# Kernel optimization log

Measured on AMD Instinct MI355X. Metric: run time of the kernel, lower is better.

## Reference

```python
import jax, jax.numpy as jnp
import numpy as np

NUM_PARAMS = 1024
BATCH = 65536


def build_lifted_core(rotation_params, diagonal_scaling_params, n):
    """Faithful translation of the torch forward's lifted-core construction."""
    h = n // 2
    dt = rotation_params.dtype
    # skew-symmetric matrix S[i,j] = r[i] - r[j]
    S = rotation_params[:, None] - rotation_params[None, :]
    I = jnp.eye(h, dtype=dt)
    # Cayley transform: (I - S)^{-1} (I + S)
    rotation = jnp.linalg.solve(I - S, I + S)
    # core = diag(d) @ rotation  (row scaling)
    core = diagonal_scaling_params[:, None] * rotation  # [h, h]
    # rot90 has period 4 in k -> precompute the 4 distinct rotated cores
    rots = jnp.stack([jnp.rot90(core, k=k) for k in range(4)])  # [4, h, h]

    def body(o, L):
        blk = jax.lax.dynamic_slice(L, (o, o), (h, h)) + rots[o % 4]
        return jax.lax.dynamic_update_slice(L, blk, (o, o))

    lifted = jax.lax.fori_loop(0, h + 1, body, jnp.zeros((n, n), dtype=dt))
    return lifted


def setup_inputs() -> dict:
    key = jax.random.key(0)
    k1, k2, k3 = jax.random.split(key, 3)
    x = jax.random.normal(k1, (BATCH, NUM_PARAMS), dtype=jnp.float32)
    rotation_params = jax.random.normal(k2, (NUM_PARAMS // 2,), dtype=jnp.float32)
    diagonal_scaling_params = jax.random.normal(k3, (NUM_PARAMS // 2,), dtype=jnp.float32)
    return {"x": x, "rotation_params": rotation_params,
            "diagonal_scaling_params": diagonal_scaling_params}


def reference(x, rotation_params, diagonal_scaling_params):
    n = x.shape[-1]
    lifted = build_lifted_core(rotation_params, diagonal_scaling_params, n)
    return x @ lifted.T
```

## Files before the change

kernel.cpp:

```cpp
#include <hip/hip_runtime.h>
#include <hip/hip_bf16.h>

typedef __attribute__((ext_vector_type(8))) short sh8;
typedef __attribute__((ext_vector_type(4))) float f32x4;
typedef unsigned short u16;
typedef unsigned int u32;

#define GLOAD16(g, l)                                                          \
  __builtin_amdgcn_global_load_lds((const __attribute__((address_space(1))) u32*)(g), \
                                   (__attribute__((address_space(3))) u32*)(l), 16, 0, 0)

__global__ __launch_bounds__(512) void prep_kernel(const float* __restrict__ r,
                                                   const float* __restrict__ d,
                                                   float* __restrict__ pq) {
  int t = threadIdx.x;
  float rv = r[t], dv = d[t];
  float s1 = rv, s2 = rv * rv;
#pragma unroll
  for (int off = 32; off; off >>= 1) {
    s1 += __shfl_down(s1, off);
    s2 += __shfl_down(s2, off);
  }
  __shared__ float a1[8], a2[8];
  if ((t & 63) == 0) { a1[t >> 6] = s1; a2[t >> 6] = s2; }
  __syncthreads();
  float S1 = 0.f, S2 = 0.f;
#pragma unroll
  for (int w = 0; w < 8; ++w) { S1 += a1[w]; S2 += a2[w]; }
  float delta = 1.f - S1 * S1 + 512.f * S2;
  float c = 2.f / delta;
  pq[t]       = c * dv * ((1.f + S1) * rv - S2);
  pq[512 + t] = -c * dv * (512.f * rv + 1.f - S1);
}

__global__ __launch_bounds__(256) void build_lifted(const float* __restrict__ rg,
                                                    const float* __restrict__ dg,
                                                    const float* __restrict__ pq,
                                                    u16* __restrict__ Lhi,
                                                    u16* __restrict__ Llo) {
  __shared__ float r[512], d[512], p[512], q[512];
  int t = threadIdx.x;
  for (int k = t; k < 512; k += 256) {
    r[k] = rg[k]; d[k] = dg[k]; p[k] = pq[k]; q[k] = pq[512 + k];
  }
  __syncthreads();
  const int i = blockIdx.x >> 2;
  const int j = ((blockIdx.x & 3) << 8) | t;
  const int olo = max(0, max(i, j) - 511);
  const int ohi = min(min(i, j), 512);
  float val = 0.f;
  for (int o = olo + ((0 - olo) & 3); o <= ohi; o += 4) {
    int a = i - o; val += p[a] + q[a] * r[j - o];
  }
  for (int o = olo + ((1 - olo) & 3); o <= ohi; o += 4) {
    int a = j - o; val += p[a] + q[a] * r[511 - i + o];
  }
  for (int o = olo + ((2 - olo) & 3); o <= ohi; o += 4) {
    int a = 511 - i + o; val += p[a] + q[a] * r[511 - j + o];
  }
  for (int o = olo + ((3 - olo) & 3); o <= ohi; o += 4) {
    int a = 511 - j + o; val += p[a] + q[a] * r[i - o];
  }
  if (i == j) {
    for (int o = olo + ((0 - olo) & 3); o <= ohi; o += 4) val += d[i - o];
    for (int o = olo + ((2 - olo) & 3); o <= ohi; o += 4) val += d[511 - i + o];
  } else if ((i + j) & 1) {
    int os = (i + j - 511) >> 1;
    if (os >= olo && os <= ohi && (os & 1)) {
      int idx = ((os & 3) == 1) ? ((511 + j - i) >> 1) : ((511 + i - j) >> 1);
      val += d[idx];
    }
  }
  __hip_bfloat16 h = __float2bfloat16(val);
  float hf = __bfloat162float(h);
  __hip_bfloat16 l = __float2bfloat16(val - hf);
  size_t idx = ((size_t)((i >> 7) * 16 + (j >> 6)) << 13) + (size_t)((i & 127) << 6) +
               (size_t)((j & 63) ^ ((i & 7) << 3));
  union { __hip_bfloat16 b; u16 u; } ch, cl;
  ch.b = h; cl.b = l;
  Lhi[idx] = ch.u; Llo[idx] = cl.u;
}

__global__ __launch_bounds__(256, 2) void gemm_kernel(const float* __restrict__ x,
                                                      const u16* __restrict__ Bhg,
                                                      const u16* __restrict__ Blg,
                                                      float* __restrict__ out) {
  __shared__ u16 Ah[8192], Al[8192], Bh[8192], Bl[8192];
  const int tid = threadIdx.x;
  const int nb = blockIdx.x & 7;
  const int mb = blockIdx.x >> 3;
  const int m0 = mb << 7;
  const int n0 = nb << 7;
  const int lane = tid & 63;
  const int wave = tid >> 6;
  const int wm = wave >> 1, wn = wave & 1;
  const int lr = lane & 15, lg = lane >> 4;
  const int sel = (lr & 7) << 3;

  const int srow = tid >> 4;
  const int scol = (tid & 15) << 2;
  const int sidx0 = (srow << 6) + (scol ^ ((srow & 7) << 3));
  const float* xbase = x + (size_t)(m0 + srow) * 1024 + scol;

  f32x4 acc[4][4] = {};
  int baseA[4], baseB[4];
#pragma unroll
  for (int f = 0; f < 4; ++f) {
    baseA[f] = ((wm << 6) + (f << 4) + lr) << 6;
    baseB[f] = ((wn << 6) + (f << 4) + lr) << 6;
  }
  const u16* tBh = Bhg + ((size_t)nb << 17);
  const u16* tBl = Blg + ((size_t)nb << 17);

  for (int kt = 0; kt < 16; ++kt) {
    __syncthreads();
    {
      const u16* gh = tBh + (kt << 13) + (tid << 3);
      const u16* gl = tBl + (kt << 13) + (tid << 3);
#pragma unroll
      for (int c = 0; c < 4; ++c) {
        GLOAD16(gh + (c << 11), &Bh[(tid << 3) + (c << 11)]);
        GLOAD16(gl + (c << 11), &Bl[(tid << 3) + (c << 11)]);
      }
    }
    float4 av[8];
    const float* xp = xbase + (kt << 6);
#pragma unroll
    for (int cc = 0; cc < 8; ++cc)
      av[cc] = *reinterpret_cast<const float4*>(xp + (size_t)cc * 16 * 1024);
#pragma unroll
    for (int cc = 0; cc < 8; ++cc) {
      float4 v = av[cc];
      __hip_bfloat162 h01 = __float22bfloat162_rn(make_float2(v.x, v.y));
      __hip_bfloat162 h23 = __float22bfloat162_rn(make_float2(v.z, v.w));
      float l0 = v.x - __bfloat162float(h01.x);
      float l1 = v.y - __bfloat162float(h01.y);
      float l2 = v.z - __bfloat162float(h23.x);
      float l3 = v.w - __bfloat162float(h23.y);
      __hip_bfloat162 m01 = __float22bfloat162_rn(make_float2(l0, l1));
      __hip_bfloat162 m23 = __float22bfloat162_rn(make_float2(l2, l3));
      union { __hip_bfloat162 h; u32 u; } uh0, uh1, ul0, ul1;
      uh0.h = h01; uh1.h = h23; ul0.h = m01; ul1.h = m23;
      int widx = sidx0 + (cc << 10);
      *reinterpret_cast<uint2*>(&Ah[widx]) = make_uint2(uh0.u, uh1.u);
      *reinterpret_cast<uint2*>(&Al[widx]) = make_uint2(ul0.u, ul1.u);
    }
    __syncthreads();
#pragma unroll
    for (int ks = 0; ks < 2; ++ks) {
      const int co = ((ks << 5) + (lg << 3)) ^ sel;
      sh8 ah[4], al[4], bh[4], bl[4];
#pragma unroll
      for (int f = 0; f < 4; ++f) {
        ah[f] = *reinterpret_cast<const sh8*>(&Ah[baseA[f] + co]);
        al[f] = *reinterpret_cast<const sh8*>(&Al[baseA[f] + co]);
        bh[f] = *reinterpret_cast<const sh8*>(&Bh[baseB[f] + co]);
        bl[f] = *reinterpret_cast<const sh8*>(&Bl[baseB[f] + co]);
      }
#pragma unroll
      for (int fm = 0; fm < 4; ++fm)
#pragma unroll
        for (int fn = 0; fn < 4; ++fn) {
          acc[fm][fn] = __builtin_amdgcn_mfma_f32_16x16x32_bf16(ah[fm], bh[fn], acc[fm][fn], 0, 0, 0);
          acc[fm][fn] = __builtin_amdgcn_mfma_f32_16x16x32_bf16(ah[fm], bl[fn], acc[fm][fn], 0, 0, 0);
          acc[fm][fn] = __builtin_amdgcn_mfma_f32_16x16x32_bf16(al[fm], bh[fn], acc[fm][fn], 0, 0, 0);
        }
    }
  }
#pragma unroll
  for (int fm = 0; fm < 4; ++fm) {
    int row = m0 + (wm << 6) + (fm << 4) + (lg << 2);
#pragma unroll
    for (int fn = 0; fn < 4; ++fn) {
      int col = n0 + (wn << 6) + (fn << 4) + lr;
      float* op = out + (size_t)row * 1024 + col;
#pragma unroll
      for (int rr = 0; rr < 4; ++rr) op[(size_t)rr * 1024] = acc[fm][fn][rr];
    }
  }
}

extern "C" void kernel_launch(void* const* d_in, const int* in_sizes, int n_in,
                              void* d_out, int out_size, void* d_ws, size_t ws_size,
                              hipStream_t stream) {
  (void)in_sizes; (void)n_in; (void)out_size; (void)ws_size;
  const float* x  = (const float*)d_in[0];
  const float* r  = (const float*)d_in[1];
  const float* dg = (const float*)d_in[2];
  float* out = (float*)d_out;
  float* pq = (float*)d_ws;
  u16* Lhi = (u16*)((char*)d_ws + 4096);
  u16* Llo = Lhi + 1024 * 1024;

  prep_kernel<<<1, 512, 0, stream>>>(r, dg, pq);
  build_lifted<<<4096, 256, 0, stream>>>(r, dg, pq, Lhi, Llo);
  gemm_kernel<<<4096, 256, 0, stream>>>(x, Lhi, Llo, out);
}
```

Baseline: 769.1 us.

## Switch GEMM to fp16 two-term split and build lifted matrix via diagonal prefix sums

The GEMM now converts x to a single fp16 value and keeps a hi/lo fp16 split only for the lifted matrix. That cuts MFMA work from three products to two per tile, drops the Al shared buffer, and raises the occupancy hint to 3 blocks. The lifted-matrix builder now runs one block per diagonal and uses shared-memory prefix sums, so each entry costs a few lookups instead of an O(n) loop. The risk is lower accuracy: x loses its low-order correction term and fp16 has a narrower range than bf16.

```diff
diff --git a/kernel.cpp b/kernel.cpp
--- a/kernel.cpp
+++ b/kernel.cpp
@@ -1,7 +1,8 @@
 #include <hip/hip_runtime.h>
 #include <hip/hip_bf16.h>
-
-typedef __attribute__((ext_vector_type(8))) short sh8;
+#include <hip/hip_fp16.h>
+
+typedef __attribute__((ext_vector_type(8))) _Float16 h8;
 typedef __attribute__((ext_vector_type(4))) float f32x4;
 typedef unsigned short u16;
 typedef unsigned int u32;
@@ -33,59 +34,119 @@
   pq[512 + t] = -c * dv * (512.f * rv + 1.f - S1);
 }
 
-__global__ __launch_bounds__(256) void build_lifted(const float* __restrict__ rg,
-                                                    const float* __restrict__ dg,
-                                                    const float* __restrict__ pq,
-                                                    u16* __restrict__ Lhi,
-                                                    u16* __restrict__ Llo) {
-  __shared__ float r[512], d[512], p[512], q[512];
-  int t = threadIdx.x;
-  for (int k = t; k < 512; k += 256) {
-    r[k] = rg[k]; d[k] = dg[k]; p[k] = pq[k]; q[k] = pq[512 + k];
+__global__ __launch_bounds__(256) void build_lifted_diag(const float* __restrict__ rg,
+                                                         const float* __restrict__ dg,
+                                                         const float* __restrict__ pq,
+                                                         u16* __restrict__ Lhi,
+                                                         u16* __restrict__ Llo) {
+  __shared__ float r_s[512], d_s[512];
+  __shared__ float W[6][512];
+  const int t = threadIdx.x;
+  const int delta = (int)blockIdx.x - 1023;
+#pragma unroll
+  for (int u = 0; u < 2; ++u) {
+    int a = t + (u << 8);
+    r_s[a] = rg[a];
+    d_s[a] = dg[a];
+    W[0][a] = pq[a];
   }
   __syncthreads();
-  const int i = blockIdx.x >> 2;
-  const int j = ((blockIdx.x & 3) << 8) | t;
-  const int olo = max(0, max(i, j) - 511);
-  const int ohi = min(min(i, j), 512);
-  float val = 0.f;
-  for (int o = olo + ((0 - olo) & 3); o <= ohi; o += 4) {
-    int a = i - o; val += p[a] + q[a] * r[j - o];
-  }
-  for (int o = olo + ((1 - olo) & 3); o <= ohi; o += 4) {
-    int a = j - o; val += p[a] + q[a] * r[511 - i + o];
-  }
-  for (int o = olo + ((2 - olo) & 3); o <= ohi; o += 4) {
-    int a = 511 - i + o; val += p[a] + q[a] * r[511 - j + o];
-  }
-  for (int o = olo + ((3 - olo) & 3); o <= ohi; o += 4) {
-    int a = 511 - j + o; val += p[a] + q[a] * r[i - o];
-  }
-  if (i == j) {
-    for (int o = olo + ((0 - olo) & 3); o <= ohi; o += 4) val += d[i - o];
-    for (int o = olo + ((2 - olo) & 3); o <= ohi; o += 4) val += d[511 - i + o];
-  } else if ((i + j) & 1) {
-    int os = (i + j - 511) >> 1;
-    if (os >= olo && os <= ohi && (os & 1)) {
-      int idx = ((os & 3) == 1) ? ((511 + j - i) >> 1) : ((511 + i - j) >> 1);
-      val += d[idx];
-    }
-  }
-  __hip_bfloat16 h = __float2bfloat16(val);
-  float hf = __bfloat162float(h);
-  __hip_bfloat16 l = __float2bfloat16(val - hf);
-  size_t idx = ((size_t)((i >> 7) * 16 + (j >> 6)) << 13) + (size_t)((i & 127) << 6) +
-               (size_t)((j & 63) ^ ((i & 7) << 3));
-  union { __hip_bfloat16 b; u16 u; } ch, cl;
-  ch.b = h; cl.b = l;
-  Lhi[idx] = ch.u; Llo[idx] = cl.u;
-}
-
-__global__ __launch_bounds__(256, 2) void gemm_kernel(const float* __restrict__ x,
+#pragma unroll
+  for (int u = 0; u < 2; ++u) {
+    int a = t + (u << 8);
+    float qa = pq[512 + a];
+    W[1][a] = d_s[a];
+    int ap = a + delta, am = a - delta;
+    int bp = 511 + delta - a, bm = 511 - delta - a;
+    W[2][a] = ((unsigned)ap < 512u) ? qa * r_s[ap] : 0.f;
+    W[3][a] = ((unsigned)am < 512u) ? qa * r_s[am] : 0.f;
+    W[4][a] = ((unsigned)bp < 512u) ? qa * r_s[bp] : 0.f;
+    W[5][a] = ((unsigned)bm < 512u) ? qa * r_s[bm] : 0.f;
+  }
+  __syncthreads();
+  float* Wf = &W[0][0];
+  for (int s = 4; s <= 256; s <<= 1) {
+    float tmp[12];
+#pragma unroll
+    for (int u = 0; u < 12; ++u) {
+      int idx = t + (u << 8);
+      tmp[u] = ((idx & 511) >= s) ? Wf[idx - s] : 0.f;
+    }
+    __syncthreads();
+#pragma unroll
+    for (int u = 0; u < 12; ++u) Wf[t + (u << 8)] += tmp[u];
+    __syncthreads();
+  }
+  const float* Pp = W[0]; const float* Pd = W[1];
+  const float* CP = W[2]; const float* CM = W[3];
+  const float* DP = W[4]; const float* DM = W[5];
+  const int imin = max(0, -delta), imax = min(1023, 1023 - delta);
+  for (int i = imin + t; i <= imax; i += 256) {
+    const int j = i + delta;
+    const int olo = max(0, max(i, j) - 511);
+    const int ohi = min(min(i, j), 512);
+    float val = 0.f;
+    {
+      int oc = olo + ((0 - olo) & 3);
+      if (oc <= ohi) {
+        int ohc = ohi - ((ohi - oc) & 3);
+        int alo = i - ohc, ahi = i - oc;
+        val += Pp[ahi] + CP[ahi];
+        if (alo >= 4) val -= Pp[alo - 4] + CP[alo - 4];
+        if (delta == 0) { val += Pd[ahi]; if (alo >= 4) val -= Pd[alo - 4]; }
+      }
+    }
+    {
+      int oc = olo + ((1 - olo) & 3);
+      if (oc <= ohi) {
+        int ohc = ohi - ((ohi - oc) & 3);
+        int alo = j - ohc, ahi = j - oc;
+        val += Pp[ahi] + DP[ahi];
+        if (alo >= 4) val -= Pp[alo - 4] + DP[alo - 4];
+      }
+    }
+    {
+      int oc = olo + ((2 - olo) & 3);
+      if (oc <= ohi) {
+        int ohc = ohi - ((ohi - oc) & 3);
+        int alo = 511 - i + oc, ahi = 511 - i + ohc;
+        val += Pp[ahi] + CM[ahi];
+        if (alo >= 4) val -= Pp[alo - 4] + CM[alo - 4];
+        if (delta == 0) { val += Pd[ahi]; if (alo >= 4) val -= Pd[alo - 4]; }
+      }
+    }
+    {
+      int oc = olo + ((3 - olo) & 3);
+      if (oc <= ohi) {
+        int ohc = ohi - ((ohi - oc) & 3);
+        int alo = 511 - j + oc, ahi = 511 - j + ohc;
+        val += Pp[ahi] + DM[ahi];
+        if (alo >= 4) val -= Pp[alo - 4] + DM[alo - 4];
+      }
+    }
+    if (delta & 1) {
+      int os = (i + j - 511) >> 1;
+      if (os >= olo && os <= ohi) {
+        int c = os & 3;
+        if (c == 1) val += d_s[j - os];
+        else if (c == 3) val += d_s[i - os];
+      }
+    }
+    __half h = __float2half(val);
+    float hf = __half2float(h);
+    __half l = __float2half(val - hf);
+    size_t idx = ((size_t)((i >> 7) * 16 + (j >> 6)) << 13) +
+                 (size_t)((i & 127) << 6) + (size_t)((j & 63) ^ ((i & 7) << 3));
+    Lhi[idx] = __half_as_ushort(h);
+    Llo[idx] = __half_as_ushort(l);
+  }
+}
+
+__global__ __launch_bounds__(256, 3) void gemm_kernel(const float* __restrict__ x,
                                                       const u16* __restrict__ Bhg,
                                                       const u16* __restrict__ Blg,
                                                       float* __restrict__ out) {
-  __shared__ u16 Ah[8192], Al[8192], Bh[8192], Bl[8192];
+  __shared__ u16 Ah[8192], Bh[8192], Bl[8192];
   const int tid = threadIdx.x;
   const int nb = blockIdx.x & 7;
   const int mb = blockIdx.x >> 3;
@@ -131,39 +192,28 @@
 #pragma unroll
     for (int cc = 0; cc < 8; ++cc) {
       float4 v = av[cc];
-      __hip_bfloat162 h01 = __float22bfloat162_rn(make_float2(v.x, v.y));
-      __hip_bfloat162 h23 = __float22bfloat162_rn(make_float2(v.z, v.w));
-      float l0 = v.x - __bfloat162float(h01.x);
-      float l1 = v.y - __bfloat162float(h01.y);
-      float l2 = v.z - __bfloat162float(h23.x);
-      float l3 = v.w - __bfloat162float(h23.y);
-      __hip_bfloat162 m01 = __float22bfloat162_rn(make_float2(l0, l1));
-      __hip_bfloat162 m23 = __float22bfloat162_rn(make_float2(l2, l3));
-      union { __hip_bfloat162 h; u32 u; } uh0, uh1, ul0, ul1;
-      uh0.h = h01; uh1.h = h23; ul0.h = m01; ul1.h = m23;
-      int widx = sidx0 + (cc << 10);
-      *reinterpret_cast<uint2*>(&Ah[widx]) = make_uint2(uh0.u, uh1.u);
-      *reinterpret_cast<uint2*>(&Al[widx]) = make_uint2(ul0.u, ul1.u);
+      union { __half2 h2[2]; uint2 u; } pk;
+      pk.h2[0] = __floats2half2_rn(v.x, v.y);
+      pk.h2[1] = __floats2half2_rn(v.z, v.w);
+      *reinterpret_cast<uint2*>(&Ah[sidx0 + (cc << 10)]) = pk.u;
     }
     __syncthreads();
 #pragma unroll
     for (int ks = 0; ks < 2; ++ks) {
       const int co = ((ks << 5) + (lg << 3)) ^ sel;
-      sh8 ah[4], al[4], bh[4], bl[4];
+      h8 ah[4], bh[4], bl[4];
 #pragma unroll
       for (int f = 0; f < 4; ++f) {
-        ah[f] = *reinterpret_cast<const sh8*>(&Ah[baseA[f] + co]);
-        al[f] = *reinterpret_cast<const sh8*>(&Al[baseA[f] + co]);
-        bh[f] = *reinterpret_cast<const sh8*>(&Bh[baseB[f] + co]);
-        bl[f] = *reinterpret_cast<const sh8*>(&Bl[baseB[f] + co]);
+        ah[f] = *reinterpret_cast<const h8*>(&Ah[baseA[f] + co]);
+        bh[f] = *reinterpret_cast<const h8*>(&Bh[baseB[f] + co]);
+        bl[f] = *reinterpret_cast<const h8*>(&Bl[baseB[f] + co]);
       }
 #pragma unroll
       for (int fm = 0; fm < 4; ++fm)
 #pragma unroll
         for (int fn = 0; fn < 4; ++fn) {
-          acc[fm][fn] = __builtin_amdgcn_mfma_f32_16x16x32_bf16(ah[fm], bh[fn], acc[fm][fn], 0, 0, 0);
-          acc[fm][fn] = __builtin_amdgcn_mfma_f32_16x16x32_bf16(ah[fm], bl[fn], acc[fm][fn], 0, 0, 0);
-          acc[fm][fn] = __builtin_amdgcn_mfma_f32_16x16x32_bf16(al[fm], bh[fn], acc[fm][fn], 0, 0, 0);
+          acc[fm][fn] = __builtin_amdgcn_mfma_f32_16x16x32_f16(ah[fm], bh[fn], acc[fm][fn], 0, 0, 0);
+          acc[fm][fn] = __builtin_amdgcn_mfma_f32_16x16x32_f16(ah[fm], bl[fn], acc[fm][fn], 0, 0, 0);
         }
     }
   }
@@ -193,6 +243,6 @@
   u16* Llo = Lhi + 1024 * 1024;
 
   prep_kernel<<<1, 512, 0, stream>>>(r, dg, pq);
-  build_lifted<<<4096, 256, 0, stream>>>(r, dg, pq, Lhi, Llo);
+  build_lifted_diag<<<2047, 256, 0, stream>>>(r, dg, pq, Lhi, Llo);
   gemm_kernel<<<4096, 256, 0, stream>>>(x, Lhi, Llo, out);
 }
```

Result: faster. 663.1 us (-13.8%).
